# Performance work log

Measured on AMD Instinct MI355X. Metric: run time of the kernel, lower is better.

## Reference

```python
import jax, jax.numpy as jnp
import numpy as np


def setup_inputs() -> dict:
    key = jax.random.key(0)
    k1, k2, k3, k4 = jax.random.split(key, 4)
    B, C, H, W = 4, 256, 64, 64
    Va = jax.random.normal(k1, (B, C, H, W), jnp.float32)
    Vb = jax.random.normal(k2, (B, C, H, W), jnp.float32)
    # nn.Linear(C, C, bias=False) weight, used as x @ W^T
    W_linear = jax.random.normal(k3, (C, C), jnp.float32) * 0.05
    # nn.Conv2d(C, 1, 1, bias=False) weight, init normal_(0, 0.01)
    W_gate = jax.random.normal(k4, (C,), jnp.float32) * 0.01
    return {"Va_output": Va, "Vb_output": Vb, "W_linear": W_linear,
            "W_gate": W_gate, "input_size": 512}


def reference(Va_output, Vb_output, W_linear, W_gate, input_size):
    B, C, H, W = Vb_output.shape
    A = H * W  # all_dim
    Va_flat = Va_output.reshape(B, C, A)  # [B, C, A]
    Vb_flat = Vb_output.reshape(B, C, A)
    # linear on transposed A-major tokens: Va_t @ W_linear^T -> [B, A, C]
    Va_corr = jnp.einsum('bca,dc->bad', Va_flat, W_linear)
    # correlation matrix S = Va_corr @ Vb_flat -> [B, A, A]
    S = jnp.einsum('bac,can->ban'[:3] + 'c,c' if False else 'bac,cn', Va_corr, Vb_flat) if False else jnp.einsum('bac,bcn->ban', Va_corr, Vb_flat)
    # S_c = softmax(S, dim=1); S_r = softmax(S^T, dim=1) = softmax(S, axis=2)^T
    S_c = jax.nn.softmax(S, axis=1)
    S_r = jnp.swapaxes(jax.nn.softmax(S, axis=2), 1, 2)
    Vb_att = jnp.einsum('bca,ban->bcn', Va_flat, S_r).reshape(B, C, H, W)
    Va_att = jnp.einsum('bca,ban->bcn', Vb_flat, S_c).reshape(B, C, H, W)
    # 1x1 gate conv (C -> 1, no bias) + sigmoid
    Va_mask = jax.nn.sigmoid(jnp.einsum('bchw,c->bhw', Va_att, W_gate))[:, None]
    Vb_mask = jax.nn.sigmoid(jnp.einsum('bchw,c->bhw', Vb_att, W_gate))[:, None]
    Va_out = jnp.concatenate([Va_att * Va_mask, Va_output], axis=1)  # [B, 2C, H, W]
    Vb_out = jnp.concatenate([Vb_att * Vb_mask, Vb_output], axis=1)
    return (Va_out, Vb_out, input_size)
```

## Files before the change

### kernel.cpp

```cpp
#include <hip/hip_runtime.h>

typedef _Float16 f16;
typedef f16 f16x8 __attribute__((ext_vector_type(8)));
typedef float f32x4 __attribute__((ext_vector_type(4)));
typedef short b16x8 __attribute__((ext_vector_type(8)));
typedef unsigned short u16;
typedef u16 u16x4 __attribute__((ext_vector_type(4)));

#define MFMA_F16(a,b,c)  __builtin_amdgcn_mfma_f32_16x16x32_f16((a),(b),(c),0,0,0)
#define MFMA_BF16(a,b,c) __builtin_amdgcn_mfma_f32_16x16x32_bf16((a),(b),(c),0,0,0)

static __device__ __forceinline__ u16 bf16rn(float f) {
    unsigned u = __builtin_bit_cast(unsigned, f);
    u += 0x7FFFu + ((u >> 16) & 1u);
    return (u16)(u >> 16);
}

typedef const __attribute__((address_space(1))) unsigned int* gas_p;
typedef __attribute__((address_space(3))) unsigned int* las_p;
static __device__ __forceinline__ void gll16(const void* g, void* l) {
    __builtin_amdgcn_global_load_lds((gas_p)g, (las_p)l, 16, 0, 0);
}

static constexpr int B_ = 4, C_ = 256, A_ = 4096;
static constexpr int CA   = C_ * A_;
static constexpr int BCA  = B_ * CA;
static constexpr int OUT_T = B_ * 2 * CA;
static constexpr size_t WS_Va16 = 0;
static constexpr size_t WS_Vb16 = WS_Va16 + (size_t)BCA;
static constexpr size_t WS_VaT  = WS_Vb16 + (size_t)BCA;
static constexpr size_t WS_VbT  = WS_VaT  + (size_t)BCA;
static constexpr size_t WS_Q1   = WS_VbT  + (size_t)BCA;
static constexpr size_t WS_W16  = WS_Q1   + (size_t)BCA;
static constexpr size_t WS_HALFS = WS_W16 + (size_t)(C_ * C_);

static constexpr float M0 = 48.0f;

__global__ void coatt_convw(const float* __restrict__ W, f16* __restrict__ W16) {
    int i = blockIdx.x * 256 + threadIdx.x;
    W16[i] = (f16)W[i];
}

__global__ void coatt_transpose(const float* __restrict__ Va,
                                const float* __restrict__ Vb,
                                u16* __restrict__ ws) {
    __shared__ f16 tile[64][72];
    int z = blockIdx.z; int b = z >> 1; int which = z & 1;
    const float* src = which ? Vb : Va;
    u16* cm = ws + (which ? WS_Vb16 : WS_Va16);
    f16* am = (f16*)(ws + (which ? WS_VbT : WS_VaT));
    int a0 = blockIdx.x * 64, c0 = blockIdx.y * 64;
    int t = threadIdx.x;
    int r = t >> 2, q = t & 3;

    const float* sp = src + (size_t)(b * C_ + c0 + r) * A_ + a0 + q * 16;
    f16 h[16] __attribute__((aligned(16)));
    u16 hb[16] __attribute__((aligned(16)));
#pragma unroll
    for (int i = 0; i < 4; ++i) {
        float4 v = *(const float4*)(sp + i * 4);
        h[i*4+0] = (f16)v.x; h[i*4+1] = (f16)v.y;
        h[i*4+2] = (f16)v.z; h[i*4+3] = (f16)v.w;
        hb[i*4+0] = bf16rn(v.x); hb[i*4+1] = bf16rn(v.y);
        hb[i*4+2] = bf16rn(v.z); hb[i*4+3] = bf16rn(v.w);
    }
    u16* cp = cm + (size_t)(b * C_ + c0 + r) * A_ + a0 + q * 16;
    *(u16x4*)(cp)      = *(const u16x4*)&hb[0];
    *(u16x4*)(cp + 4)  = *(const u16x4*)&hb[4];
    *(u16x4*)(cp + 8)  = *(const u16x4*)&hb[8];
    *(u16x4*)(cp + 12) = *(const u16x4*)&hb[12];
#pragma unroll
    for (int i = 0; i < 16; ++i) tile[r][q * 16 + i] = h[i];
    __syncthreads();
    f16 ht[16] __attribute__((aligned(16)));
#pragma unroll
    for (int i = 0; i < 16; ++i) ht[i] = tile[q * 16 + i][r];
    f16* ap = am + (size_t)(b * A_ + a0 + r) * C_ + c0 + q * 16;
    *(f16x8*)(ap)     = *(const f16x8*)&ht[0];
    *(f16x8*)(ap + 8) = *(const f16x8*)&ht[8];
}

__global__ __launch_bounds__(256) void coatt_q1(const f16* __restrict__ vat,
                                                const f16* __restrict__ w16,
                                                f16* __restrict__ q1) {
    int b = blockIdx.y; int a0 = blockIdx.x * 64;
    int tid = threadIdx.x, wave = tid >> 6, lane = tid & 63;
    int m = lane & 15, quad = lane >> 4;

    const f16* Ap = vat + (size_t)(b * A_ + a0 + wave * 16 + m) * C_ + quad * 8;
    f16x8 af[8];
#pragma unroll
    for (int kc = 0; kc < 8; ++kc) af[kc] = *(const f16x8*)(Ap + kc * 32);

    f32x4 acc[16];
#pragma unroll
    for (int t = 0; t < 16; ++t) acc[t] = (f32x4){0.f, 0.f, 0.f, 0.f};

#pragma unroll
    for (int kc = 0; kc < 8; ++kc) {
#pragma unroll
        for (int t = 0; t < 16; ++t) {
            f16x8 bf = *(const f16x8*)(w16 + (size_t)(t * 16 + m) * C_ + kc * 32 + quad * 8);
            acc[t] = MFMA_F16(af[kc], bf, acc[t]);
        }
    }
#pragma unroll
    for (int t = 0; t < 16; ++t) {
#pragma unroll
        for (int r = 0; r < 4; ++r) {
            int arow = a0 + wave * 16 + quad * 4 + r;
            q1[(size_t)(b * A_ + arow) * C_ + t * 16 + m] = (f16)acc[t][r];
        }
    }
}

__global__ __launch_bounds__(256, 2) void coatt_flash(const u16* __restrict__ ws,
                                                      const float* __restrict__ Wgate,
                                                      float* __restrict__ dout) {
    __shared__ __align__(16) char smem[74752];
    char* Klds = smem;
    char* Vlds = smem + 32768;
    char* Plds = smem + 65536;
    float* Olds = (float*)smem;
    float* Lsum = (float*)(smem + 65536);
    float* Gsum = (float*)(smem + 65536 + 512);

    int att = blockIdx.z, b = blockIdx.y;
    int n0 = blockIdx.x * 64;
    const f16 *Qp, *Kp; const u16* Vp; float* outp;
    if (att == 0) {
        Qp = (const f16*)(ws + WS_Q1)  + (size_t)b * CA;
        Kp = (const f16*)(ws + WS_VbT) + (size_t)b * CA;
        Vp = ws + WS_Va16 + (size_t)b * CA;
        outp = dout + (size_t)OUT_T + (size_t)b * 2 * CA;
    } else {
        Qp = (const f16*)(ws + WS_VbT) + (size_t)b * CA;
        Kp = (const f16*)(ws + WS_Q1)  + (size_t)b * CA;
        Vp = ws + WS_Vb16 + (size_t)b * CA;
        outp = dout + (size_t)b * 2 * CA;
    }

    int tid = threadIdx.x, wave = tid >> 6, lane = tid & 63;
    int i = wave >> 1, j = wave & 1;
    int m = lane & 15, quad = lane >> 4;

    f16x8 qf[2][8];
#pragma unroll
    for (int qt = 0; qt < 2; ++qt) {
        const f16* qr = Qp + (size_t)(n0 + i * 32 + qt * 16 + m) * C_ + quad * 8;
#pragma unroll
        for (int kc = 0; kc < 8; ++kc) qf[qt][kc] = *(const f16x8*)(qr + kc * 32);
    }

    f32x4 Oacc[2][8];
#pragma unroll
    for (int qt = 0; qt < 2; ++qt)
#pragma unroll
        for (int ct = 0; ct < 8; ++ct) Oacc[qt][ct] = (f32x4){0.f, 0.f, 0.f, 0.f};
    float lpart[2] = {0.f, 0.f};

    int krl = 2 * wave + (lane >> 5);
    int kch = (lane & 31) ^ krl;
    int vcl = lane >> 3;
    int vch = (lane & 7) ^ vcl;

    for (int kb = 0; kb < 64; ++kb) {
        int key0 = kb * 64;
        {
            const f16* kg = Kp + (size_t)(key0 + krl) * C_ + kch * 8;
            char* kl = Klds + wave * 1024;
#pragma unroll
            for (int ii = 0; ii < 8; ++ii)
                gll16(kg + ii * 2048, kl + ii * 4096);
            const u16* vg = Vp + (size_t)(wave * 8 + vcl) * A_ + key0 + vch * 8;
            char* vl = Vlds + wave * 1024;
#pragma unroll
            for (int ii = 0; ii < 8; ++ii)
                gll16(vg + (size_t)ii * 32 * A_, vl + ii * 4096);
        }
        __syncthreads();

        f32x4 Sc[2][2];
#pragma unroll
        for (int kt = 0; kt < 2; ++kt)
#pragma unroll
            for (int qt = 0; qt < 2; ++qt) Sc[kt][qt] = (f32x4){0.f, 0.f, 0.f, 0.f};
#pragma unroll
        for (int kc = 0; kc < 8; ++kc) {
            f16x8 kf[2];
#pragma unroll
            for (int kt = 0; kt < 2; ++kt) {
                int kl_ = j * 32 + kt * 16 + m;
                kf[kt] = *(const f16x8*)(Klds + kl_ * 512 +
                                         (((kc * 4 + quad) ^ (kl_ & 7)) << 4));
            }
#pragma unroll
            for (int kt = 0; kt < 2; ++kt)
#pragma unroll
                for (int qt = 0; qt < 2; ++qt)
                    Sc[kt][qt] = MFMA_F16(kf[kt], qf[qt][kc], Sc[kt][qt]);
        }

#pragma unroll
        for (int qt = 0; qt < 2; ++qt) {
            int qg = i * 32 + qt * 16 + m;
#pragma unroll
            for (int kt = 0; kt < 2; ++kt) {
                u16x4 pk;
                float s4 = 0.f;
#pragma unroll
                for (int r = 0; r < 4; ++r) {
                    float p = __expf(Sc[kt][qt][r] - M0);
                    s4 += p;
                    pk[r] = bf16rn(p);
                }
                lpart[qt] += s4;
                *(u16x4*)(Plds + qg * 144 + (j * 32 + kt * 16 + quad * 4) * 2) = pk;
            }
        }
        __syncthreads();

#pragma unroll
        for (int kt = 0; kt < 2; ++kt) {
            b16x8 pf[2];
#pragma unroll
            for (int qt = 0; qt < 2; ++qt) {
                int qg = i * 32 + qt * 16 + m;
                pf[qt] = *(const b16x8*)(Plds + qg * 144 + kt * 64 + quad * 16);
            }
#pragma unroll
            for (int ct = 0; ct < 8; ++ct) {
                int c = j * 128 + ct * 16 + m;
                b16x8 vf = *(const b16x8*)(Vlds + c * 128 +
                                           (((kt * 4 + quad) ^ (c & 7)) << 4));
#pragma unroll
                for (int qt = 0; qt < 2; ++qt)
                    Oacc[qt][ct] = MFMA_BF16(pf[qt], vf, Oacc[qt][ct]);
            }
        }
        __syncthreads();
    }

#pragma unroll
    for (int qt = 0; qt < 2; ++qt) {
        float v = lpart[qt];
        v += __shfl_xor(v, 16);
        v += __shfl_xor(v, 32);
        lpart[qt] = v;
    }
    if (lane < 16) {
#pragma unroll
        for (int qt = 0; qt < 2; ++qt)
            Lsum[j * 64 + i * 32 + qt * 16 + lane] = lpart[qt];
    }
    __syncthreads();
    float inv[2][4];
#pragma unroll
    for (int qt = 0; qt < 2; ++qt)
#pragma unroll
        for (int r = 0; r < 4; ++r) {
            int q = i * 32 + qt * 16 + quad * 4 + r;
            inv[qt][r] = 1.0f / (Lsum[q] + Lsum[64 + q]);
        }
    float gp[2][4] = {{0.f,0.f,0.f,0.f},{0.f,0.f,0.f,0.f}};
#pragma unroll
    for (int ct = 0; ct < 8; ++ct) {
        float w = Wgate[j * 128 + ct * 16 + m];
#pragma unroll
        for (int qt = 0; qt < 2; ++qt)
#pragma unroll
            for (int r = 0; r < 4; ++r) {
                float o = Oacc[qt][ct][r] * inv[qt][r];
                Oacc[qt][ct][r] = o;
                gp[qt][r] += o * w;
            }
    }
#pragma unroll
    for (int qt = 0; qt < 2; ++qt)
#pragma unroll
        for (int r = 0; r < 4; ++r) {
            float v = gp[qt][r];
            v += __shfl_xor(v, 1); v += __shfl_xor(v, 2);
            v += __shfl_xor(v, 4); v += __shfl_xor(v, 8);
            gp[qt][r] = v;
        }
    if (m == 0) {
#pragma unroll
        for (int qt = 0; qt < 2; ++qt)
#pragma unroll
            for (int r = 0; r < 4; ++r)
                Gsum[j * 64 + i * 32 + qt * 16 + quad * 4 + r] = gp[qt][r];
    }
    __syncthreads();
#pragma unroll
    for (int qt = 0; qt < 2; ++qt)
#pragma unroll
        for (int r = 0; r < 4; ++r) {
            int q = i * 32 + qt * 16 + quad * 4 + r;
            float g = Gsum[q] + Gsum[64 + q];
            float msk = 1.0f / (1.0f + __expf(-g));
#pragma unroll
            for (int ct = 0; ct < 8; ++ct) Oacc[qt][ct][r] *= msk;
        }

    for (int hf = 0; hf < 2; ++hf) {
        __syncthreads();
        if (j == hf) {
#pragma unroll
            for (int ct = 0; ct < 8; ++ct)
#pragma unroll
                for (int qt = 0; qt < 2; ++qt)
#pragma unroll
                    for (int r = 0; r < 4; ++r)
                        Olds[(ct * 16 + m) * 68 + i * 32 + qt * 16 + quad * 4 + r] =
                            Oacc[qt][ct][r];
        }
        __syncthreads();
#pragma unroll
        for (int ii = 0; ii < 8; ++ii) {
            int ci = tid + ii * 256;
            int c = ci >> 4, ch = (ci & 15) * 4;
            float4 v = *(const float4*)(Olds + c * 68 + ch);
            *(float4*)(outp + (size_t)(hf * 128 + c) * A_ + n0 + ch) = v;
        }
    }
}

__global__ void coatt_copy(const float* __restrict__ Va, const float* __restrict__ Vb,
                           const int* __restrict__ psz, float* __restrict__ dout) {
    int base = blockIdx.x * 256 + threadIdx.x;
    const float4* va4 = (const float4*)Va;
    const float4* vb4 = (const float4*)Vb;
    float4* out4 = (float4*)dout;
#pragma unroll
    for (int i = 0; i < 4; ++i) {
        int idx = base + i * 524288;
        int t = idx >> 20;
        int r = idx & 1048575;
        int b = r >> 18;
        int rr = r & 262143;
        float4 v = t ? vb4[r] : va4[r];
        out4[(size_t)t * 2097152 + (size_t)b * 524288 + 262144 + rr] = v;
    }
    if (base == 0) dout[16777216] = (float)(*psz);
}

extern "C" void kernel_launch(void* const* d_in, const int* in_sizes, int n_in,
                              void* d_out, int out_size, void* d_ws, size_t ws_size,
                              hipStream_t stream) {
    const float* Va = (const float*)d_in[0];
    const float* Vb = (const float*)d_in[1];
    const float* Wl = (const float*)d_in[2];
    const float* Wg = (const float*)d_in[3];
    const int* psz  = (const int*)d_in[4];
    float* out = (float*)d_out;
    u16* ws = (u16*)d_ws;

    if (ws_size < WS_HALFS * sizeof(u16)) return;

    coatt_convw<<<256, 256, 0, stream>>>(Wl, (f16*)(ws + WS_W16));
    coatt_transpose<<<dim3(64, 4, 8), 256, 0, stream>>>(Va, Vb, ws);
    coatt_q1<<<dim3(64, 4), 256, 0, stream>>>((const f16*)(ws + WS_VaT),
                                              (const f16*)(ws + WS_W16),
                                              (f16*)(ws + WS_Q1));
    coatt_flash<<<dim3(64, 4, 2), 256, 0, stream>>>(ws, Wg, out);
    coatt_copy<<<2048, 256, 0, stream>>>(Va, Vb, psz, out);
}
```

Measured before the change: 288.9 us.

## Double-buffer K/V tiles and widen flash blocks to 128 queries

The flash co-attention kernel now runs 512-thread blocks that each cover 128 queries instead of 64, so every K/V tile fetched into LDS serves twice as many queries. The next K and V tiles are prefetched into a second LDS buffer with global_load_lds while the current tile is being computed, which also removes the trailing barrier of each loop iteration. The grid is flattened so that neighbouring blocks spread across batch and attention direction. In exchange, LDS use rises to about 148 KB per block, so each CU holds one large block rather than two smaller ones, and the epilogue buffers are re-laid out for 128 columns.

Measured after the change: 271.0 us. 1.07x faster.

```diff
diff --git a/kernel.cpp b/kernel.cpp
--- a/kernel.cpp
+++ b/kernel.cpp
@@ -114,19 +114,20 @@
     }
 }
 
-__global__ __launch_bounds__(256, 2) void coatt_flash(const u16* __restrict__ ws,
+__global__ __launch_bounds__(512, 2) void coatt_flash(const u16* __restrict__ ws,
                                                       const float* __restrict__ Wgate,
                                                       float* __restrict__ dout) {
-    __shared__ __align__(16) char smem[74752];
-    char* Klds = smem;
-    char* Vlds = smem + 32768;
-    char* Plds = smem + 65536;
+    __shared__ __align__(16) char smem[151552];
+    char* Plds = smem + 131072;
+    float* Lsum = (float*)(smem + 149504);
+    float* Gsum = (float*)(smem + 150528);
     float* Olds = (float*)smem;
-    float* Lsum = (float*)(smem + 65536);
-    float* Gsum = (float*)(smem + 65536 + 512);
-
-    int att = blockIdx.z, b = blockIdx.y;
-    int n0 = blockIdx.x * 64;
+
+    int p = blockIdx.x;
+    int vc = p & 7;
+    int b = vc & 3, att = vc >> 2;
+    int n0 = (p >> 3) * 128;
+
     const f16 *Qp, *Kp; const u16* Vp; float* outp;
     if (att == 0) {
         Qp = (const f16*)(ws + WS_Q1)  + (size_t)b * CA;
@@ -159,26 +160,34 @@
         for (int ct = 0; ct < 8; ++ct) Oacc[qt][ct] = (f32x4){0.f, 0.f, 0.f, 0.f};
     float lpart[2] = {0.f, 0.f};
 
-    int krl = 2 * wave + (lane >> 5);
-    int kch = (lane & 31) ^ krl;
-    int vcl = lane >> 3;
-    int vch = (lane & 7) ^ vcl;
+    int kch = (lane & 31) ^ ((2 * wave + (lane >> 5)) & 7);
+    int vch = (lane & 7) ^ ((lane >> 3) & 7);
+    const f16* kgb = Kp + (size_t)(2 * wave + (lane >> 5)) * C_ + kch * 8;
+    const u16* vgb = Vp + (size_t)(8 * wave + (lane >> 3)) * A_ + vch * 8;
+
+    {
+        const f16* kg = kgb;
+        char* kl = smem + wave * 1024;
+#pragma unroll
+        for (int ii = 0; ii < 4; ++ii) gll16(kg + ii * 16 * C_, kl + ii * 8192);
+        const u16* vg = vgb;
+        char* vl = smem + 65536 + wave * 1024;
+#pragma unroll
+        for (int ii = 0; ii < 4; ++ii) gll16(vg + (size_t)ii * 64 * A_, vl + ii * 8192);
+    }
 
     for (int kb = 0; kb < 64; ++kb) {
-        int key0 = kb * 64;
-        {
-            const f16* kg = Kp + (size_t)(key0 + krl) * C_ + kch * 8;
-            char* kl = Klds + wave * 1024;
-#pragma unroll
-            for (int ii = 0; ii < 8; ++ii)
-                gll16(kg + ii * 2048, kl + ii * 4096);
-            const u16* vg = Vp + (size_t)(wave * 8 + vcl) * A_ + key0 + vch * 8;
-            char* vl = Vlds + wave * 1024;
-#pragma unroll
-            for (int ii = 0; ii < 8; ++ii)
-                gll16(vg + (size_t)ii * 32 * A_, vl + ii * 4096);
-        }
+        int cur = kb & 1, nxt = cur ^ 1;
+        char* Kc = smem + cur * 32768;
+        char* Vc = smem + 65536 + cur * 32768;
         __syncthreads();
+
+        if (kb < 63) {
+            const f16* kg = kgb + (size_t)(kb + 1) * 64 * C_;
+            char* kl = smem + nxt * 32768 + wave * 1024;
+#pragma unroll
+            for (int ii = 0; ii < 4; ++ii) gll16(kg + ii * 16 * C_, kl + ii * 8192);
+        }
 
         f32x4 Sc[2][2];
 #pragma unroll
@@ -191,7 +200,7 @@
 #pragma unroll
             for (int kt = 0; kt < 2; ++kt) {
                 int kl_ = j * 32 + kt * 16 + m;
-                kf[kt] = *(const f16x8*)(Klds + kl_ * 512 +
+                kf[kt] = *(const f16x8*)(Kc + kl_ * 512 +
                                          (((kc * 4 + quad) ^ (kl_ & 7)) << 4));
             }
 #pragma unroll
@@ -210,9 +219,9 @@
                 float s4 = 0.f;
 #pragma unroll
                 for (int r = 0; r < 4; ++r) {
-                    float p = __expf(Sc[kt][qt][r] - M0);
-                    s4 += p;
-                    pk[r] = bf16rn(p);
+                    float pv = __expf(Sc[kt][qt][r] - M0);
+                    s4 += pv;
+                    pk[r] = bf16rn(pv);
                 }
                 lpart[qt] += s4;
                 *(u16x4*)(Plds + qg * 144 + (j * 32 + kt * 16 + quad * 4) * 2) = pk;
@@ -220,6 +229,13 @@
         }
         __syncthreads();
 
+        if (kb < 63) {
+            const u16* vg = vgb + (size_t)(kb + 1) * 64;
+            char* vl = smem + 65536 + nxt * 32768 + wave * 1024;
+#pragma unroll
+            for (int ii = 0; ii < 4; ++ii) gll16(vg + (size_t)ii * 64 * A_, vl + ii * 8192);
+        }
+
 #pragma unroll
         for (int kt = 0; kt < 2; ++kt) {
             b16x8 pf[2];
@@ -231,14 +247,13 @@
 #pragma unroll
             for (int ct = 0; ct < 8; ++ct) {
                 int c = j * 128 + ct * 16 + m;
-                b16x8 vf = *(const b16x8*)(Vlds + c * 128 +
+                b16x8 vf = *(const b16x8*)(Vc + c * 128 +
                                            (((kt * 4 + quad) ^ (c & 7)) << 4));
 #pragma unroll
                 for (int qt = 0; qt < 2; ++qt)
                     Oacc[qt][ct] = MFMA_BF16(pf[qt], vf, Oacc[qt][ct]);
             }
         }
-        __syncthreads();
     }
 
 #pragma unroll
@@ -248,10 +263,11 @@
         v += __shfl_xor(v, 32);
         lpart[qt] = v;
     }
+    __syncthreads();
     if (lane < 16) {
 #pragma unroll
         for (int qt = 0; qt < 2; ++qt)
-            Lsum[j * 64 + i * 32 + qt * 16 + lane] = lpart[qt];
+            Lsum[j * 128 + i * 32 + qt * 16 + lane] = lpart[qt];
     }
     __syncthreads();
     float inv[2][4];
@@ -260,7 +276,7 @@
 #pragma unroll
         for (int r = 0; r < 4; ++r) {
             int q = i * 32 + qt * 16 + quad * 4 + r;
-            inv[qt][r] = 1.0f / (Lsum[q] + Lsum[64 + q]);
+            inv[qt][r] = 1.0f / (Lsum[q] + Lsum[128 + q]);
         }
     float gp[2][4] = {{0.f,0.f,0.f,0.f},{0.f,0.f,0.f,0.f}};
 #pragma unroll
@@ -289,7 +305,7 @@
         for (int qt = 0; qt < 2; ++qt)
 #pragma unroll
             for (int r = 0; r < 4; ++r)
-                Gsum[j * 64 + i * 32 + qt * 16 + quad * 4 + r] = gp[qt][r];
+                Gsum[j * 128 + i * 32 + qt * 16 + quad * 4 + r] = gp[qt][r];
     }
     __syncthreads();
 #pragma unroll
@@ -297,7 +313,7 @@
 #pragma unroll
         for (int r = 0; r < 4; ++r) {
             int q = i * 32 + qt * 16 + quad * 4 + r;
-            float g = Gsum[q] + Gsum[64 + q];
+            float g = Gsum[q] + Gsum[128 + q];
             float msk = 1.0f / (1.0f + __expf(-g));
 #pragma unroll
             for (int ct = 0; ct < 8; ++ct) Oacc[qt][ct][r] *= msk;
@@ -312,15 +328,15 @@
                 for (int qt = 0; qt < 2; ++qt)
 #pragma unroll
                     for (int r = 0; r < 4; ++r)
-                        Olds[(ct * 16 + m) * 68 + i * 32 + qt * 16 + quad * 4 + r] =
+                        Olds[(ct * 16 + m) * 132 + i * 32 + qt * 16 + quad * 4 + r] =
                             Oacc[qt][ct][r];
         }
         __syncthreads();
 #pragma unroll
         for (int ii = 0; ii < 8; ++ii) {
-            int ci = tid + ii * 256;
-            int c = ci >> 4, ch = (ci & 15) * 4;
-            float4 v = *(const float4*)(Olds + c * 68 + ch);
+            int ci = tid + ii * 512;
+            int c = ci >> 5, ch = (ci & 31) * 4;
+            float4 v = *(const float4*)(Olds + c * 132 + ch);
             *(float4*)(outp + (size_t)(hf * 128 + c) * A_ + n0 + ch) = v;
         }
     }
@@ -363,6 +379,6 @@
     coatt_q1<<<dim3(64, 4), 256, 0, stream>>>((const f16*)(ws + WS_VaT),
                                               (const f16*)(ws + WS_W16),
                                               (f16*)(ws + WS_Q1));
-    coatt_flash<<<dim3(64, 4, 2), 256, 0, stream>>>(ws, Wg, out);
+    coatt_flash<<<256, 512, 0, stream>>>(ws, Wg, out);
     coatt_copy<<<2048, 256, 0, stream>>>(Va, Vb, psz, out);
 }
```
